# Kernel optimization log

Measured on AMD Instinct MI355X. Metric: run time of the kernel, lower is better.

The kernel has to match this reference:

```python
import jax, jax.numpy as jnp
import numpy as np

B, T, H = 64, 4096, 1024
SCALE = 1.0 / np.sqrt(H).astype(np.float32)


def setup_inputs() -> dict:
    key = jax.random.key(0)
    k1, k2 = jax.random.split(key)
    dec_h = jax.random.normal(k1, (B, H), dtype=jnp.float32)
    enc_out = jax.random.normal(k2, (B, T, H), dtype=jnp.float32)
    return {"dec_h": dec_h, "enc_out": enc_out}


def reference(dec_h, enc_out):
    # scores: [B, T] = enc_out @ dec_h (per-batch GEMV), scaled
    scores = jnp.einsum("bth,bh->bt", enc_out, dec_h) * SCALE
    weights = jax.nn.softmax(scores, axis=1)              # [B, T]
    ctx = jnp.einsum("bt,bth->bh", weights, enc_out)      # [B, H]
    return (ctx, weights)
```

## Files before the change

### kernel.cpp

```cpp
#include <hip/hip_runtime.h>
#include <math.h>

namespace {

constexpr int B = 64;
constexpr int T = 4096;
constexpr int H = 1024;
constexpr float SCALE = 0.03125f;
constexpr int WPB = 4;

__global__ __launch_bounds__(256) void attn_pass1(
    const float* __restrict__ dec_h, const float* __restrict__ enc,
    float* __restrict__ scores, float* __restrict__ acc_ws,
    float* __restrict__ ml_ws, int chunks, int rows_per_wave) {
  const int b = blockIdx.y;
  const int chunk = blockIdx.x;
  const int wave = threadIdx.x >> 6;
  const int lane = threadIdx.x & 63;
  const int wslot = chunk * WPB + wave;
  const int t0 = wslot * rows_per_wave;

  const float* decb = dec_h + (size_t)b * H + lane * 4;
  const float4 d0 = *(const float4*)(decb + 0 * 256);
  const float4 d1 = *(const float4*)(decb + 1 * 256);
  const float4 d2 = *(const float4*)(decb + 2 * 256);
  const float4 d3 = *(const float4*)(decb + 3 * 256);

  float4 a0 = {0.f, 0.f, 0.f, 0.f}, a1 = {0.f, 0.f, 0.f, 0.f};
  float4 a2 = {0.f, 0.f, 0.f, 0.f}, a3 = {0.f, 0.f, 0.f, 0.f};
  float m = -INFINITY;
  float l = 0.f;

  const float* row = enc + ((size_t)b * T + t0) * H + lane * 4;
  float* srow = scores + (size_t)b * T + t0;

#pragma unroll 2
  for (int r = 0; r < rows_per_wave; ++r) {
    const float4 x0 = *(const float4*)(row + 0 * 256);
    const float4 x1 = *(const float4*)(row + 1 * 256);
    const float4 x2 = *(const float4*)(row + 2 * 256);
    const float4 x3 = *(const float4*)(row + 3 * 256);
    row += H;

    float s;
    s  = x0.x * d0.x + x0.y * d0.y + x0.z * d0.z + x0.w * d0.w;
    s += x1.x * d1.x + x1.y * d1.y + x1.z * d1.z + x1.w * d1.w;
    s += x2.x * d2.x + x2.y * d2.y + x2.z * d2.z + x2.w * d2.w;
    s += x3.x * d3.x + x3.y * d3.y + x3.z * d3.z + x3.w * d3.w;
#pragma unroll
    for (int off = 32; off > 0; off >>= 1) s += __shfl_xor(s, off, 64);
    s *= SCALE;

    if (lane == 0) srow[r] = s;

    if (s > m) {
      const float sc = __expf(m - s);
      a0.x *= sc; a0.y *= sc; a0.z *= sc; a0.w *= sc;
      a1.x *= sc; a1.y *= sc; a1.z *= sc; a1.w *= sc;
      a2.x *= sc; a2.y *= sc; a2.z *= sc; a2.w *= sc;
      a3.x *= sc; a3.y *= sc; a3.z *= sc; a3.w *= sc;
      l *= sc;
      m = s;
    }
    const float p = __expf(s - m);
    l += p;
    a0.x += p * x0.x; a0.y += p * x0.y; a0.z += p * x0.z; a0.w += p * x0.w;
    a1.x += p * x1.x; a1.y += p * x1.y; a1.z += p * x1.z; a1.w += p * x1.w;
    a2.x += p * x2.x; a2.y += p * x2.y; a2.z += p * x2.z; a2.w += p * x2.w;
    a3.x += p * x3.x; a3.y += p * x3.y; a3.z += p * x3.z; a3.w += p * x3.w;
  }

  const size_t pi = (size_t)b * chunks * WPB + wslot;
  float* aw = acc_ws + pi * H + lane * 4;
  *(float4*)(aw + 0 * 256) = a0;
  *(float4*)(aw + 1 * 256) = a1;
  *(float4*)(aw + 2 * 256) = a2;
  *(float4*)(aw + 3 * 256) = a3;
  if (lane == 0) {
    ml_ws[2 * pi]     = m;
    ml_ws[2 * pi + 1] = l;
  }
}

__global__ __launch_bounds__(256) void attn_pass2(
    const float* __restrict__ acc_ws, const float* __restrict__ ml_ws,
    float* __restrict__ ctx, float* __restrict__ weights, int np) {
  const int b = blockIdx.x;
  const int tid = threadIdx.x;
  const float* ml = ml_ws + 2 * (size_t)b * np;

  float M = -INFINITY;
  for (int i = 0; i < np; ++i) M = fmaxf(M, ml[2 * i]);
  float L = 0.f;
  for (int i = 0; i < np; ++i) L += ml[2 * i + 1] * __expf(ml[2 * i] - M);
  const float invL = 1.f / L;

  float4 a = {0.f, 0.f, 0.f, 0.f};
  const float* aw = acc_ws + (size_t)b * np * H + tid * 4;
  for (int i = 0; i < np; ++i) {
    const float w = __expf(ml[2 * i] - M);
    const float4 v = *(const float4*)(aw + (size_t)i * H);
    a.x += w * v.x; a.y += w * v.y; a.z += w * v.z; a.w += w * v.w;
  }
  a.x *= invL; a.y *= invL; a.z *= invL; a.w *= invL;
  *(float4*)(ctx + (size_t)b * H + tid * 4) = a;

  float* wrow = weights + (size_t)b * T;
  for (int t = tid; t < T; t += 256) {
    wrow[t] = __expf(wrow[t] - M) * invL;
  }
}

}

extern "C" void kernel_launch(void* const* d_in, const int* in_sizes, int n_in,
                              void* d_out, int out_size, void* d_ws,
                              size_t ws_size, hipStream_t stream) {
  const float* dec_h = (const float*)d_in[0];
  const float* enc   = (const float*)d_in[1];
  float* ctx     = (float*)d_out;
  float* weights = (float*)d_out + (size_t)B * H;

  int chunks = 16;
  while (chunks > 1 &&
         (size_t)B * chunks * WPB * (H + 2) * sizeof(float) > ws_size)
    chunks >>= 1;
  const int rows_per_wave = T / (chunks * WPB);
  const int np = chunks * WPB;

  float* acc_ws = (float*)d_ws;
  float* ml_ws  = acc_ws + (size_t)B * np * H;

  dim3 g1(chunks, B);
  attn_pass1<<<g1, 256, 0, stream>>>(dec_h, enc, weights, acc_ws, ml_ws,
                                     chunks, rows_per_wave);
  attn_pass2<<<B, 256, 0, stream>>>(acc_ws, ml_ws, ctx, weights, np);
}
```

Baseline: 230.3 us.

## Software-prefetch next row with nontemporal loads and batch score stores

The pass-1 loop now loads the next encoder row into registers while computing the current one, so the load of row r+1 overlaps the reduction and softmax update of row r. Encoder reads use nontemporal loads because the data streams through once. Per-row scalar score stores from lane 0 are replaced by collecting 64 scores across lanes and writing them in one coalesced store. Code is also switched to ext_vector_type arithmetic, and register pressure goes up from the extra row buffer. The batched store assumes rows per wave is a multiple of 64.

```diff
diff --git a/kernel.cpp b/kernel.cpp
--- a/kernel.cpp
+++ b/kernel.cpp
@@ -9,73 +9,83 @@
 constexpr float SCALE = 0.03125f;
 constexpr int WPB = 4;
 
+typedef float v4f __attribute__((ext_vector_type(4)));
+
 __global__ __launch_bounds__(256) void attn_pass1(
     const float* __restrict__ dec_h, const float* __restrict__ enc,
     float* __restrict__ scores, float* __restrict__ acc_ws,
-    float* __restrict__ ml_ws, int chunks, int rows_per_wave) {
+    float* __restrict__ ml_ws, int chunks, int rpw) {
   const int b = blockIdx.y;
-  const int chunk = blockIdx.x;
   const int wave = threadIdx.x >> 6;
   const int lane = threadIdx.x & 63;
-  const int wslot = chunk * WPB + wave;
-  const int t0 = wslot * rows_per_wave;
+  const int wslot = blockIdx.x * WPB + wave;
+  const int t0 = wslot * rpw;
 
   const float* decb = dec_h + (size_t)b * H + lane * 4;
-  const float4 d0 = *(const float4*)(decb + 0 * 256);
-  const float4 d1 = *(const float4*)(decb + 1 * 256);
-  const float4 d2 = *(const float4*)(decb + 2 * 256);
-  const float4 d3 = *(const float4*)(decb + 3 * 256);
+  const v4f d0 = *(const v4f*)(decb);
+  const v4f d1 = *(const v4f*)(decb + 256);
+  const v4f d2 = *(const v4f*)(decb + 512);
+  const v4f d3 = *(const v4f*)(decb + 768);
 
-  float4 a0 = {0.f, 0.f, 0.f, 0.f}, a1 = {0.f, 0.f, 0.f, 0.f};
-  float4 a2 = {0.f, 0.f, 0.f, 0.f}, a3 = {0.f, 0.f, 0.f, 0.f};
+  v4f a0 = {0.f, 0.f, 0.f, 0.f}, a1 = {0.f, 0.f, 0.f, 0.f};
+  v4f a2 = {0.f, 0.f, 0.f, 0.f}, a3 = {0.f, 0.f, 0.f, 0.f};
   float m = -INFINITY;
   float l = 0.f;
+  float sv = 0.f;
 
-  const float* row = enc + ((size_t)b * T + t0) * H + lane * 4;
+  const v4f* rp = (const v4f*)(enc + ((size_t)b * T + t0) * H) + lane;
   float* srow = scores + (size_t)b * T + t0;
 
-#pragma unroll 2
-  for (int r = 0; r < rows_per_wave; ++r) {
-    const float4 x0 = *(const float4*)(row + 0 * 256);
-    const float4 x1 = *(const float4*)(row + 1 * 256);
-    const float4 x2 = *(const float4*)(row + 2 * 256);
-    const float4 x3 = *(const float4*)(row + 3 * 256);
-    row += H;
+  v4f x0 = __builtin_nontemporal_load(rp);
+  v4f x1 = __builtin_nontemporal_load(rp + 64);
+  v4f x2 = __builtin_nontemporal_load(rp + 128);
+  v4f x3 = __builtin_nontemporal_load(rp + 192);
 
-    float s;
-    s  = x0.x * d0.x + x0.y * d0.y + x0.z * d0.z + x0.w * d0.w;
-    s += x1.x * d1.x + x1.y * d1.y + x1.z * d1.z + x1.w * d1.w;
-    s += x2.x * d2.x + x2.y * d2.y + x2.z * d2.z + x2.w * d2.w;
-    s += x3.x * d3.x + x3.y * d3.y + x3.z * d3.z + x3.w * d3.w;
+  for (int r = 0; r < rpw; ++r) {
+    v4f y0, y1, y2, y3;
+    if (r + 1 < rpw) {
+      const v4f* rq = rp + 256;
+      y0 = __builtin_nontemporal_load(rq);
+      y1 = __builtin_nontemporal_load(rq + 64);
+      y2 = __builtin_nontemporal_load(rq + 128);
+      y3 = __builtin_nontemporal_load(rq + 192);
+    }
+    rp += 256;
+
+    float sA = x0[0] * d0[0] + x0[1] * d0[1] + x0[2] * d0[2] + x0[3] * d0[3];
+    float sB = x1[0] * d1[0] + x1[1] * d1[1] + x1[2] * d1[2] + x1[3] * d1[3];
+    sA += x2[0] * d2[0] + x2[1] * d2[1] + x2[2] * d2[2] + x2[3] * d2[3];
+    sB += x3[0] * d3[0] + x3[1] * d3[1] + x3[2] * d3[2] + x3[3] * d3[3];
+    float s = sA + sB;
 #pragma unroll
     for (int off = 32; off > 0; off >>= 1) s += __shfl_xor(s, off, 64);
     s *= SCALE;
 
-    if (lane == 0) srow[r] = s;
+    sv = (lane == (r & 63)) ? s : sv;
+    if ((r & 63) == 63) srow[(r & ~63) + lane] = sv;
 
     if (s > m) {
       const float sc = __expf(m - s);
-      a0.x *= sc; a0.y *= sc; a0.z *= sc; a0.w *= sc;
-      a1.x *= sc; a1.y *= sc; a1.z *= sc; a1.w *= sc;
-      a2.x *= sc; a2.y *= sc; a2.z *= sc; a2.w *= sc;
-      a3.x *= sc; a3.y *= sc; a3.z *= sc; a3.w *= sc;
+      a0 *= sc; a1 *= sc; a2 *= sc; a3 *= sc;
       l *= sc;
       m = s;
     }
     const float p = __expf(s - m);
     l += p;
-    a0.x += p * x0.x; a0.y += p * x0.y; a0.z += p * x0.z; a0.w += p * x0.w;
-    a1.x += p * x1.x; a1.y += p * x1.y; a1.z += p * x1.z; a1.w += p * x1.w;
-    a2.x += p * x2.x; a2.y += p * x2.y; a2.z += p * x2.z; a2.w += p * x2.w;
-    a3.x += p * x3.x; a3.y += p * x3.y; a3.z += p * x3.z; a3.w += p * x3.w;
+    a0 += p * x0;
+    a1 += p * x1;
+    a2 += p * x2;
+    a3 += p * x3;
+
+    x0 = y0; x1 = y1; x2 = y2; x3 = y3;
   }
 
   const size_t pi = (size_t)b * chunks * WPB + wslot;
   float* aw = acc_ws + pi * H + lane * 4;
-  *(float4*)(aw + 0 * 256) = a0;
-  *(float4*)(aw + 1 * 256) = a1;
-  *(float4*)(aw + 2 * 256) = a2;
-  *(float4*)(aw + 3 * 256) = a3;
+  *(v4f*)(aw)       = a0;
+  *(v4f*)(aw + 256) = a1;
+  *(v4f*)(aw + 512) = a2;
+  *(v4f*)(aw + 768) = a3;
   if (lane == 0) {
     ml_ws[2 * pi]     = m;
     ml_ws[2 * pi + 1] = l;
@@ -95,15 +105,15 @@
   for (int i = 0; i < np; ++i) L += ml[2 * i + 1] * __expf(ml[2 * i] - M);
   const float invL = 1.f / L;
 
-  float4 a = {0.f, 0.f, 0.f, 0.f};
+  v4f a = {0.f, 0.f, 0.f, 0.f};
   const float* aw = acc_ws + (size_t)b * np * H + tid * 4;
   for (int i = 0; i < np; ++i) {
     const float w = __expf(ml[2 * i] - M);
-    const float4 v = *(const float4*)(aw + (size_t)i * H);
-    a.x += w * v.x; a.y += w * v.y; a.z += w * v.z; a.w += w * v.w;
+    const v4f v = *(const v4f*)(aw + (size_t)i * H);
+    a += w * v;
   }
-  a.x *= invL; a.y *= invL; a.z *= invL; a.w *= invL;
-  *(float4*)(ctx + (size_t)b * H + tid * 4) = a;
+  a *= invL;
+  *(v4f*)(ctx + (size_t)b * H + tid * 4) = a;
 
   float* wrow = weights + (size_t)b * T;
   for (int t = tid; t < T; t += 256) {
@@ -125,7 +135,7 @@
   while (chunks > 1 &&
          (size_t)B * chunks * WPB * (H + 2) * sizeof(float) > ws_size)
     chunks >>= 1;
-  const int rows_per_wave = T / (chunks * WPB);
+  const int rpw = T / (chunks * WPB);
   const int np = chunks * WPB;
 
   float* acc_ws = (float*)d_ws;
@@ -133,6 +143,6 @@
 
   dim3 g1(chunks, B);
   attn_pass1<<<g1, 256, 0, stream>>>(dec_h, enc, weights, acc_ws, ml_ws,
-                                     chunks, rows_per_wave);
+                                     chunks, rpw);
   attn_pass2<<<B, 256, 0, stream>>>(acc_ws, ml_ws, ctx, weights, np);
 }
```

Measured after the change: 207.8 us (median of 2 runs). -9.8%, faster.
